# Kernel tuning notes

Hardware: AMD Instinct MI355X
Metric: run time of the kernel (lower is better)

Reference implementation:

```python
import jax, jax.numpy as jnp
import numpy as np

N, E = 50000, 800000
IN_DIM, EDGE_DIM, HID, OUT_DIM, L = 128, 16, 64, 8, 4
MSG_EPS = 1e-7  # GENConv eps added to relu(msg)


def layer_norm(x, g, b, eps=1e-5):
    mu = x.mean(-1, keepdims=True)
    var = ((x - mu) ** 2).mean(-1, keepdims=True)
    return (x - mu) * jax.lax.rsqrt(var + eps) * g + b


def segment_softmax(logits, seg, num_segments):
    # numerically stable softmax over edges grouped by destination node
    m = jax.ops.segment_max(logits, seg, num_segments=num_segments)
    m = jnp.where(jnp.isfinite(m), m, 0.0)
    e = jnp.exp(logits - m[seg])
    s = jax.ops.segment_sum(e, seg, num_segments=num_segments)
    return e / (s[seg] + 1e-16)


def gen_conv(x, src, dst, ea, t, W1, b1, g1, be1, W2, b2):
    # GENConv: message = relu(x_j + e_ij) + eps, softmax-aggregate by dst, add root, MLP [h->2h->h]
    msg = jax.nn.relu(x[src] + ea) + MSG_EPS          # [E, H]
    alpha = segment_softmax(msg * t, dst, x.shape[0]) # [E, H]
    agg = jax.ops.segment_sum(msg * alpha, dst, num_segments=x.shape[0])  # [N, H]
    h = agg + x
    h = jax.nn.relu(layer_norm(h @ W1 + b1, g1, be1))  # [N, 2H]
    return h @ W2 + b2                                 # [N, H]


def setup_inputs() -> dict:
    key = jax.random.key(0)
    ks = jax.random.split(key, 16)
    sc = 0.05
    inp = {
        "x": jax.random.normal(ks[0], (N, IN_DIM), jnp.float32),
        "edge_attr": jax.random.normal(ks[1], (E, EDGE_DIM), jnp.float32),
        "node_W": jax.random.normal(ks[2], (IN_DIM, HID), jnp.float32) * sc,
        "node_b": jnp.zeros((HID,), jnp.float32),
        "edge_W": jax.random.normal(ks[3], (EDGE_DIM, HID), jnp.float32) * sc,
        "edge_b": jnp.zeros((HID,), jnp.float32),
        "conv_t": jnp.ones((L,), jnp.float32),
        "conv_W1": jax.random.normal(ks[4], (L, HID, 2 * HID), jnp.float32) * sc,
        "conv_b1": jnp.zeros((L, 2 * HID), jnp.float32),
        "conv_g1": jnp.ones((L, 2 * HID), jnp.float32),
        "conv_be1": jnp.zeros((L, 2 * HID), jnp.float32),
        "conv_W2": jax.random.normal(ks[5], (L, 2 * HID, HID), jnp.float32) * sc,
        "conv_b2": jnp.zeros((L, HID), jnp.float32),
        "ln_g": jnp.ones((L, HID), jnp.float32),
        "ln_b": jnp.zeros((L, HID), jnp.float32),
        "lin_W": jax.random.normal(ks[6], (HID, OUT_DIM), jnp.float32) * sc,
        "lin_b": jnp.zeros((OUT_DIM,), jnp.float32),
        "edge_index": jax.random.randint(ks[7], (2, E), 0, N, jnp.int64),
    }
    return inp


def reference(x, edge_attr, node_W, node_b, edge_W, edge_b,
              conv_t, conv_W1, conv_b1, conv_g1, conv_be1, conv_W2, conv_b2,
              ln_g, ln_b, lin_W, lin_b, edge_index):
    src, dst = edge_index[0], edge_index[1]  # flow: source_to_target
    h = x @ node_W + node_b
    ea = edge_attr @ edge_W + edge_b
    # first layer: conv only (DeeperGCN applies layers[0].conv directly)
    h = gen_conv(h, src, dst, ea, conv_t[0], conv_W1[0], conv_b1[0],
                 conv_g1[0], conv_be1[0], conv_W2[0], conv_b2[0])
    # res+ blocks: x + conv(dropout(relu(norm(x)))); dropout inactive (eval)
    for i in range(1, L):
        z = jax.nn.relu(layer_norm(h, ln_g[i], ln_b[i]))
        h = h + gen_conv(z, src, dst, ea, conv_t[i], conv_W1[i], conv_b1[i],
                         conv_g1[i], conv_be1[i], conv_W2[i], conv_b2[i])
    h = jax.nn.relu(layer_norm(h, ln_g[0], ln_b[0]))
    return h @ lin_W + lin_b
```

## Files before the change

### kernel.cpp

```cpp
#include <hip/hip_runtime.h>
#include <hip/hip_fp16.h>

#define N_NODES 50000
#define N_EDGES 800000
#define IN_DIM  128
#define EDGE_DIM 16
#define HID     64
#define HID2    128
#define OUT_DIM 8
#define N_LAYERS 4
#define NBUCK   391
#define CCHUNK  4096
#define CBLOCKS 196

typedef _Float16 half8 __attribute__((ext_vector_type(8)));
typedef float floatx4 __attribute__((ext_vector_type(4)));

static __device__ __forceinline__ float bcast(float v, int l) {
    return __uint_as_float(__builtin_amdgcn_readlane(__float_as_uint(v), l));
}

__global__ __launch_bounds__(256, 4) void chist_kernel(
    const int* __restrict__ dsts, int* __restrict__ ccnt)
{
    __shared__ int lh[NBUCK];
    for (int i = threadIdx.x; i < NBUCK; i += 256) lh[i] = 0;
    __syncthreads();
    const int base = blockIdx.x * CCHUNK;
#pragma unroll
    for (int i = 0; i < 16; ++i) {
        const int e = base + i * 256 + threadIdx.x;
        if (e < N_EDGES) atomicAdd(&lh[dsts[e] >> 7], 1);
    }
    __syncthreads();
    for (int i = threadIdx.x; i < NBUCK; i += 256)
        if (lh[i]) atomicAdd(&ccnt[i], lh[i]);
}

__global__ __launch_bounds__(256, 1) void cscan_kernel(
    const int* __restrict__ ccnt, int* __restrict__ coff, int* __restrict__ ccur)
{
    __shared__ int part[512];
    const int t = threadIdx.x;
    part[t]       = (t < NBUCK)       ? ccnt[t]       : 0;
    part[t + 256] = (t + 256 < NBUCK) ? ccnt[t + 256] : 0;
    __syncthreads();
    for (int off = 1; off < 512; off <<= 1) {
        const int v0 = (t >= off) ? part[t - off] : 0;
        const int v1 = (t + 256 >= off) ? part[t + 256 - off] : 0;
        __syncthreads();
        part[t] += v0; part[t + 256] += v1;
        __syncthreads();
    }
    if (t < NBUCK) { const int ex = (t > 0) ? part[t - 1] : 0; coff[t] = ex; ccur[t] = ex; }
    const int i2 = t + 256;
    if (i2 < NBUCK) { coff[i2] = part[i2 - 1]; ccur[i2] = part[i2 - 1]; }
    if (t == 0) coff[NBUCK] = part[NBUCK - 1];
}

__global__ __launch_bounds__(256, 4) void cscatter_kernel(
    const int* __restrict__ srcs, const int* __restrict__ dsts,
    int* __restrict__ ccur, uint2* __restrict__ tmp)
{
    __shared__ int lh[NBUCK], lbase[NBUCK], lrank[NBUCK];
    for (int i = threadIdx.x; i < NBUCK; i += 256) { lh[i] = 0; lrank[i] = 0; }
    __syncthreads();
    const int base = blockIdx.x * CCHUNK;
    int myd[16], mys[16];
#pragma unroll
    for (int i = 0; i < 16; ++i) {
        const int e = base + i * 256 + threadIdx.x;
        if (e < N_EDGES) {
            myd[i] = dsts[e]; mys[i] = srcs[e];
            atomicAdd(&lh[myd[i] >> 7], 1);
        } else myd[i] = -1;
    }
    __syncthreads();
    for (int i = threadIdx.x; i < NBUCK; i += 256) {
        const int c = lh[i];
        lbase[i] = c ? atomicAdd(&ccur[i], c) : 0;
    }
    __syncthreads();
#pragma unroll
    for (int i = 0; i < 16; ++i) {
        if (myd[i] >= 0) {
            const int e = base + i * 256 + threadIdx.x;
            const int b = myd[i] >> 7;
            const int r = atomicAdd(&lrank[b], 1);
            tmp[lbase[b] + r] =
                make_uint2((unsigned)mys[i] | ((unsigned)myd[i] << 16),
                           (unsigned)e);
        }
    }
}

__global__ __launch_bounds__(256, 1) void fsort_kernel(
    const uint2* __restrict__ tmp, const int* __restrict__ coff,
    unsigned* __restrict__ sd2, int* __restrict__ eid)
{
    __shared__ uint2 ebuf[4096];
    __shared__ int lh[128], lsc[128];
    const int b = blockIdx.x;
    const int lo = coff[b];
    const int cnt = coff[b + 1] - lo;
    if (threadIdx.x < 128) lh[threadIdx.x] = 0;
    __syncthreads();
    for (int i = threadIdx.x; i < cnt; i += 256) {
        const uint2 v = tmp[lo + i];
        ebuf[i] = v;
        atomicAdd(&lh[(int)(v.x >> 16) - b * 128], 1);
    }
    __syncthreads();
    if (threadIdx.x < 128) lsc[threadIdx.x] = lh[threadIdx.x];
    __syncthreads();
    for (int off = 1; off < 128; off <<= 1) {
        int v = 0;
        if (threadIdx.x < 128 && threadIdx.x >= off) v = lsc[threadIdx.x - off];
        __syncthreads();
        if (threadIdx.x < 128) lsc[threadIdx.x] += v;
        __syncthreads();
    }
    if (threadIdx.x < 128) lh[threadIdx.x] = lsc[threadIdx.x] - lh[threadIdx.x];
    __syncthreads();
    for (int i = threadIdx.x; i < cnt; i += 256) {
        const uint2 v = ebuf[i];
        const int d = (int)(v.x >> 16) - b * 128;
        const int pos = atomicAdd(&lh[d], 1);
        sd2[lo + pos] = v.x;
        eid[lo + pos] = (int)v.y;
    }
}

__global__ __launch_bounds__(256, 2) void node_proj_kernel(
    const float* __restrict__ x, const float* __restrict__ W,
    const float* __restrict__ b, float* __restrict__ h, __half* __restrict__ zh)
{
    __shared__ float xs[4][IN_DIM];
    const int c = threadIdx.x & 63;
    const int local_n = threadIdx.x >> 6;
    float w[IN_DIM];
#pragma unroll
    for (int k = 0; k < IN_DIM; ++k) w[k] = W[k * HID + c];
    const float bias = b[c];

    for (int base = blockIdx.x * 4; base < N_NODES; base += gridDim.x * 4) {
        __syncthreads();
#pragma unroll
        for (int i = 0; i < 2; ++i) {
            int idx = threadIdx.x + i * 256;
            int nn = idx >> 7, kk = idx & 127;
            xs[nn][kk] = x[(base + nn) * IN_DIM + kk];
        }
        __syncthreads();
        const int n = base + local_n;
        float acc = bias;
#pragma unroll
        for (int k4 = 0; k4 < IN_DIM / 4; ++k4) {
            float4 xv = ((const float4*)xs[local_n])[k4];
            acc = fmaf(xv.x, w[k4 * 4 + 0], acc);
            acc = fmaf(xv.y, w[k4 * 4 + 1], acc);
            acc = fmaf(xv.z, w[k4 * 4 + 2], acc);
            acc = fmaf(xv.w, w[k4 * 4 + 3], acc);
        }
        h[n * HID + c] = acc;
        zh[n * HID + c] = __float2half(acc);
    }
}

__global__ __launch_bounds__(256, 4) void edge_emb_kernel(
    const float* __restrict__ ea, const float* __restrict__ W,
    const float* __restrict__ b, const int* __restrict__ eid,
    __half* __restrict__ eah)
{
    __shared__ __half lds_t[4][16 * HID];
    const int lane = threadIdx.x & 63;
    const int waveid = threadIdx.x >> 6;
    const int wave = (blockIdx.x * 256 + threadIdx.x) >> 6;
    const int nwaves = gridDim.x * 4;
    const int m = lane & 15, q = lane >> 4;
    const int NT = N_EDGES / 16;

    half8 bf[4];
#pragma unroll
    for (int blk = 0; blk < 4; ++blk) {
#pragma unroll
        for (int i = 0; i < 8; ++i) {
            const int k = q * 8 + i;
            bf[blk][i] = (k < EDGE_DIM)
                ? (_Float16)W[k * HID + blk * 16 + m] : (_Float16)0.f;
        }
    }
    float bv[4];
#pragma unroll
    for (int blk = 0; blk < 4; ++blk) bv[blk] = b[blk * 16 + m];

    const int ed = lane >> 3, ch = lane & 7;

    for (int tile = wave; tile < NT; tile += nwaves) {
        const int e0 = tile * 16;
        const int eidx = eid[e0 + m];
        half8 af;
#pragma unroll
        for (int i = 0; i < 8; ++i) af[i] = (_Float16)0.f;
        if (q < 2) {
            const float4* ap =
                (const float4*)(ea + (size_t)eidx * EDGE_DIM + q * 8);
            const float4 lo = ap[0];
            const float4 hi = ap[1];
            af[0] = (_Float16)lo.x; af[1] = (_Float16)lo.y;
            af[2] = (_Float16)lo.z; af[3] = (_Float16)lo.w;
            af[4] = (_Float16)hi.x; af[5] = (_Float16)hi.y;
            af[6] = (_Float16)hi.z; af[7] = (_Float16)hi.w;
        }
        floatx4 c[4];
#pragma unroll
        for (int blk = 0; blk < 4; ++blk) {
            floatx4 cin = {bv[blk], bv[blk], bv[blk], bv[blk]};
            c[blk] = __builtin_amdgcn_mfma_f32_16x16x32_f16(
                af, bf[blk], cin, 0, 0, 0);
        }
#pragma unroll
        for (int blk = 0; blk < 4; ++blk)
#pragma unroll
            for (int r = 0; r < 4; ++r)
                lds_t[waveid][(q * 4 + r) * HID + blk * 16 + m] =
                    __float2half(c[blk][r]);
        const float4 v0 =
            *(const float4*)&lds_t[waveid][ed * HID + ch * 8];
        const float4 v1 =
            *(const float4*)&lds_t[waveid][(8 + ed) * HID + ch * 8];
        ((float4*)(eah + (size_t)(e0 + ed) * HID))[ch] = v0;
        ((float4*)(eah + (size_t)(e0 + 8 + ed) * HID))[ch] = v1;
    }
}

__global__ __launch_bounds__(256, 3) void edge_agg_kernel(
    const __half* __restrict__ zh, const __half* __restrict__ eah,
    const unsigned* __restrict__ sd2,
    const float* __restrict__ conv_t, int layer,
    float2* __restrict__ ps)
{
    const int lane = threadIdx.x & 63;
    const int wave = (blockIdx.x * 256 + threadIdx.x) >> 6;
    const int nwaves = gridDim.x * 4;
    const float t2 = conv_t[layer] * 1.4426950408889634f;
    const int NT = N_EDGES / 64;

    const _Float16* zf = (const _Float16*)zh;
    const _Float16* ef = (const _Float16*)eah;

    for (int tile = wave; tile < NT; tile += nwaves) {
        const int e0 = tile * 64;
        const unsigned sdv = sd2[e0 + lane];
        const _Float16* erow = ef + (size_t)e0 * HID + lane;

        _Float16 ez[64];
#pragma unroll
        for (int k = 0; k < 64; ++k) ez[k] = erow[(size_t)k * HID];

        const int sv = (int)(sdv & 0xffffu);
        const int dv = (int)(sdv >> 16);
        const int pv = __shfl_up(dv, 1, 64);
        const unsigned long long bmask = __ballot(dv != pv) & ~1ull;

        _Float16 za[16], zb[16];
#pragma unroll
        for (int k = 0; k < 16; ++k) {
            const int a = __builtin_amdgcn_readlane(sv, k);
            za[k] = zf[(size_t)a * HID + lane];
        }

        float S = 0.f, P = 0.f;
        int cur = __builtin_amdgcn_readlane(dv, 0);
        bool first = true;
#pragma unroll
        for (int g = 0; g < 4; ++g) {
            if (g < 3) {
#pragma unroll
                for (int k = 0; k < 16; ++k) {
                    const int a = __builtin_amdgcn_readlane(sv, (g + 1) * 16 + k);
                    zb[k] = zf[(size_t)a * HID + lane];
                }
            }
#pragma unroll
            for (int k = 0; k < 16; ++k) {
                const int j = g * 16 + k;
                if (bmask & (1ull << j)) {
                    float2* addr = &ps[(size_t)cur * HID + lane];
                    if (first) {
                        unsafeAtomicAdd(&addr->x, P);
                        unsafeAtomicAdd(&addr->y, S);
                        first = false;
                    } else {
                        *addr = make_float2(P, S);
                    }
                    S = 0.f; P = 0.f;
                    cur = __builtin_amdgcn_readlane(dv, j);
                }
                _Float16 mh = za[k] + ez[j];
                mh = mh > (_Float16)0.f ? mh : (_Float16)0.f;
                const float mm = (float)mh + 1e-7f;
                const float xx = __builtin_amdgcn_exp2f(mm * t2);
                S += xx;
                P = fmaf(mm, xx, P);
            }
            if (g < 3) {
#pragma unroll
                for (int k = 0; k < 16; ++k) za[k] = zb[k];
            }
        }
        {
            float2* addr = &ps[(size_t)cur * HID + lane];
            unsafeAtomicAdd(&addr->x, P);
            unsafeAtomicAdd(&addr->y, S);
        }
    }
}

__global__ __launch_bounds__(256, 3) void node_mm1_kernel(
    float2* __restrict__ ps,
    const __half* __restrict__ zh,
    const float* __restrict__ W1, const float* __restrict__ b1,
    const float* __restrict__ g1, const float* __restrict__ be1,
    __half* __restrict__ vh)
{
    const int lane = threadIdx.x & 63;
    const int wave = (blockIdx.x * 256 + threadIdx.x) >> 6;

    float wa[HID], wb[HID];
#pragma unroll
    for (int k = 0; k < HID; ++k) {
        wa[k] = W1[k * HID2 + lane];
        wb[k] = W1[k * HID2 + 64 + lane];
    }
    const float ba = b1[lane],  bb = b1[64 + lane];
    const float ga = g1[lane],  gb = g1[64 + lane];
    const float ca = be1[lane], cb = be1[64 + lane];

    int idx[4];
    float2 pv[4];
    float zv[4];
#pragma unroll
    for (int i = 0; i < 4; ++i) idx[i] = (wave + i * 12500) * HID + lane;
#pragma unroll
    for (int i = 0; i < 4; ++i) pv[i] = ps[idx[i]];
#pragma unroll
    for (int i = 0; i < 4; ++i) zv[i] = __half2float(zh[idx[i]]);
#pragma unroll
    for (int i = 0; i < 4; ++i) ps[idx[i]] = make_float2(0.f, 0.f);
    float hv[4];
#pragma unroll
    for (int i = 0; i < 4; ++i)
        hv[i] = pv[i].x / (pv[i].y + 1e-16f) + zv[i];

#pragma unroll
    for (int pr = 0; pr < 2; ++pr) {
        const float h0 = hv[pr * 2], h1 = hv[pr * 2 + 1];
        float a0 = 0.f, a1 = 0.f, c0 = 0.f, c1 = 0.f;
        float d0 = 0.f, d1 = 0.f, e0 = 0.f, e1 = 0.f;
#pragma unroll
        for (int k = 0; k < 32; ++k) {
            const float x0 = bcast(h0, k);
            const float x1 = bcast(h0, k + 32);
            const float y0 = bcast(h1, k);
            const float y1 = bcast(h1, k + 32);
            a0 = fmaf(x0, wa[k], a0);
            c0 = fmaf(x0, wb[k], c0);
            a1 = fmaf(x1, wa[k + 32], a1);
            c1 = fmaf(x1, wb[k + 32], c1);
            d0 = fmaf(y0, wa[k], d0);
            e0 = fmaf(y0, wb[k], e0);
            d1 = fmaf(y1, wa[k + 32], d1);
            e1 = fmaf(y1, wb[k + 32], e1);
        }
        const float ua0 = (a0 + a1) + ba, ub0 = (c0 + c1) + bb;
        const float ua1 = (d0 + d1) + ba, ub1 = (e0 + e1) + bb;

        float s0 = ua0 + ub0, s1 = ua1 + ub1;
#pragma unroll
        for (int o = 1; o < 64; o <<= 1) {
            s0 += __shfl_xor(s0, o, 64);
            s1 += __shfl_xor(s1, o, 64);
        }
        const float mu0 = s0 * (1.f / 128.f), mu1 = s1 * (1.f / 128.f);
        const float da0 = ua0 - mu0, db0 = ub0 - mu0;
        const float da1 = ua1 - mu1, db1 = ub1 - mu1;
        float q0 = fmaf(da0, da0, db0 * db0);
        float q1 = fmaf(da1, da1, db1 * db1);
#pragma unroll
        for (int o = 1; o < 64; o <<= 1) {
            q0 += __shfl_xor(q0, o, 64);
            q1 += __shfl_xor(q1, o, 64);
        }
        const float r0 = rsqrtf(q0 * (1.f / 128.f) + 1e-5f);
        const float r1 = rsqrtf(q1 * (1.f / 128.f) + 1e-5f);
        const float ya0 = da0 * r0 * ga + ca, yb0 = db0 * r0 * gb + cb;
        const float ya1 = da1 * r1 * ga + ca, yb1 = db1 * r1 * gb + cb;
        const size_t v0 = (size_t)(wave + pr * 2 * 12500) * HID2;
        const size_t v1 = (size_t)(wave + (pr * 2 + 1) * 12500) * HID2;
        vh[v0 + lane]      = __float2half(ya0 > 0.f ? ya0 : 0.f);
        vh[v0 + 64 + lane] = __float2half(yb0 > 0.f ? yb0 : 0.f);
        vh[v1 + lane]      = __float2half(ya1 > 0.f ? ya1 : 0.f);
        vh[v1 + 64 + lane] = __float2half(yb1 > 0.f ? yb1 : 0.f);
    }
}

__global__ __launch_bounds__(256, 3) void node_mm2_kernel(
    const __half* __restrict__ vh,
    const float* __restrict__ W2, const float* __restrict__ b2,
    const float* __restrict__ lng, const float* __restrict__ lnb,
    float* __restrict__ h, __half* __restrict__ zh, int residual)
{
    const int lane = threadIdx.x & 63;
    const int wave = (blockIdx.x * 256 + threadIdx.x) >> 6;

    float wa[HID], wb[HID];
#pragma unroll
    for (int k = 0; k < HID; ++k) {
        wa[k] = W2[k * HID + lane];
        wb[k] = W2[(k + 64) * HID + lane];
    }
    const float bias = b2[lane];
    const float g = lng[lane];
    const float be = lnb[lane];

    int idx[4];
    float f0[4], f1[4], hold[4];
#pragma unroll
    for (int i = 0; i < 4; ++i) idx[i] = (wave + i * 12500) * HID + lane;
#pragma unroll
    for (int i = 0; i < 4; ++i) {
        const size_t vb = (size_t)(wave + i * 12500) * HID2;
        f0[i] = __half2float(vh[vb + lane]);
        f1[i] = __half2float(vh[vb + 64 + lane]);
    }
#pragma unroll
    for (int i = 0; i < 4; ++i) hold[i] = h[idx[i]];

#pragma unroll
    for (int pr = 0; pr < 2; ++pr) {
        const int i0 = pr * 2, i1 = pr * 2 + 1;
        float a0 = 0.f, a1 = 0.f, c0 = 0.f, c1 = 0.f;
        float d0 = 0.f, d1 = 0.f, e0 = 0.f, e1 = 0.f;
#pragma unroll
        for (int k = 0; k < 32; ++k) {
            a0 = fmaf(bcast(f0[i0], k),      wa[k],      a0);
            a1 = fmaf(bcast(f0[i0], k + 32), wa[k + 32], a1);
            c0 = fmaf(bcast(f1[i0], k),      wb[k],      c0);
            c1 = fmaf(bcast(f1[i0], k + 32), wb[k + 32], c1);
            d0 = fmaf(bcast(f0[i1], k),      wa[k],      d0);
            d1 = fmaf(bcast(f0[i1], k + 32), wa[k + 32], d1);
            e0 = fmaf(bcast(f1[i1], k),      wb[k],      e0);
            e1 = fmaf(bcast(f1[i1], k + 32), wb[k + 32], e1);
        }
        const float acc0 = (a0 + a1) + (c0 + c1) + bias;
        const float acc1 = (d0 + d1) + (e0 + e1) + bias;
        const float hn0 = residual ? (hold[i0] + acc0) : acc0;
        const float hn1 = residual ? (hold[i1] + acc1) : acc1;
        h[idx[i0]] = hn0;
        h[idx[i1]] = hn1;

        float s0 = hn0, s1 = hn1;
#pragma unroll
        for (int o = 1; o < 64; o <<= 1) {
            s0 += __shfl_xor(s0, o, 64);
            s1 += __shfl_xor(s1, o, 64);
        }
        const float mu0 = s0 * (1.f / 64.f), mu1 = s1 * (1.f / 64.f);
        const float dd0 = hn0 - mu0, dd1 = hn1 - mu1;
        float q0 = dd0 * dd0, q1 = dd1 * dd1;
#pragma unroll
        for (int o = 1; o < 64; o <<= 1) {
            q0 += __shfl_xor(q0, o, 64);
            q1 += __shfl_xor(q1, o, 64);
        }
        const float r0 = rsqrtf(q0 * (1.f / 64.f) + 1e-5f);
        const float r1 = rsqrtf(q1 * (1.f / 64.f) + 1e-5f);
        const float y0 = dd0 * r0 * g + be;
        const float y1 = dd1 * r1 * g + be;
        zh[idx[i0]] = __float2half(y0 > 0.f ? y0 : 0.f);
        zh[idx[i1]] = __float2half(y1 > 0.f ? y1 : 0.f);
    }
}

__global__ __launch_bounds__(256, 4) void final_kernel(
    const __half* __restrict__ zh, const float* __restrict__ Wl,
    const float* __restrict__ bl, float* __restrict__ out)
{
    __shared__ float wl[HID * OUT_DIM];
    for (int i = threadIdx.x; i < HID * OUT_DIM; i += 256) wl[i] = Wl[i];
    __syncthreads();
    const int total = N_NODES * OUT_DIM;
    for (int idx = blockIdx.x * 256 + threadIdx.x; idx < total;
         idx += gridDim.x * 256) {
        const int n = idx >> 3, o = idx & 7;
        const __half2* zp = (const __half2*)(zh + (size_t)n * HID);
        float acc = bl[o];
#pragma unroll
        for (int k2 = 0; k2 < HID / 2; ++k2) {
            const float2 f = __half22float2(zp[k2]);
            acc = fmaf(f.x, wl[(k2 * 2 + 0) * OUT_DIM + o], acc);
            acc = fmaf(f.y, wl[(k2 * 2 + 1) * OUT_DIM + o], acc);
        }
        out[idx] = acc;
    }
}

extern "C" void kernel_launch(void* const* d_in, const int* in_sizes, int n_in,
                              void* d_out, int out_size, void* d_ws, size_t ws_size,
                              hipStream_t stream)
{
    const float* x         = (const float*)d_in[0];
    const float* edge_attr = (const float*)d_in[1];
    const float* node_W    = (const float*)d_in[2];
    const float* node_b    = (const float*)d_in[3];
    const float* edge_W    = (const float*)d_in[4];
    const float* edge_b    = (const float*)d_in[5];
    const float* conv_t    = (const float*)d_in[6];
    const float* conv_W1   = (const float*)d_in[7];
    const float* conv_b1   = (const float*)d_in[8];
    const float* conv_g1   = (const float*)d_in[9];
    const float* conv_be1  = (const float*)d_in[10];
    const float* conv_W2   = (const float*)d_in[11];
    const float* conv_b2   = (const float*)d_in[12];
    const float* ln_g      = (const float*)d_in[13];
    const float* ln_b      = (const float*)d_in[14];
    const float* lin_W     = (const float*)d_in[15];
    const float* lin_b     = (const float*)d_in[16];
    const int*   edge_index= (const int*)d_in[17];
    const int*   srcs = edge_index;
    const int*   dsts = edge_index + N_EDGES;
    float* out = (float*)d_out;

    float* h    = (float*)d_ws;
    float2* ps  = (float2*)(h + N_NODES * HID);
    __half* vh  = (__half*)(ps + N_NODES * HID);
    __half* zh  = vh + (size_t)N_NODES * HID2;
    __half* eah = zh + (size_t)N_NODES * HID;
    uint2* tmp  = (uint2*)(eah + (size_t)N_EDGES * HID);
    unsigned* sd2 = (unsigned*)(tmp + N_EDGES);
    int* eid    = (int*)(sd2 + N_EDGES);
    int* ccnt   = eid + N_EDGES;
    int* coff   = ccnt + NBUCK;
    int* ccur   = coff + NBUCK + 1;

    hipMemsetAsync(ccnt, 0, (size_t)NBUCK * sizeof(int), stream);
    chist_kernel<<<CBLOCKS, 256, 0, stream>>>(dsts, ccnt);
    cscan_kernel<<<1, 256, 0, stream>>>(ccnt, coff, ccur);
    cscatter_kernel<<<CBLOCKS, 256, 0, stream>>>(srcs, dsts, ccur, tmp);
    fsort_kernel<<<NBUCK, 256, 0, stream>>>(tmp, coff, sd2, eid);

    node_proj_kernel<<<2048, 256, 0, stream>>>(x, node_W, node_b, h, zh);
    edge_emb_kernel<<<3125, 256, 0, stream>>>(edge_attr, edge_W, edge_b, eid, eah);

    hipMemsetAsync(ps, 0, (size_t)N_NODES * HID * sizeof(float2), stream);

    for (int layer = 0; layer < N_LAYERS; ++layer) {
        edge_agg_kernel<<<3125, 256, 0, stream>>>(zh, eah, sd2,
                                                  conv_t, layer, ps);
        node_mm1_kernel<<<3125, 256, 0, stream>>>(
            ps, zh,
            conv_W1 + (size_t)layer * HID * HID2, conv_b1 + layer * HID2,
            conv_g1 + layer * HID2, conv_be1 + layer * HID2, vh);
        const float* gz = (layer < N_LAYERS - 1) ? (ln_g + (layer + 1) * HID) : ln_g;
        const float* bz = (layer < N_LAYERS - 1) ? (ln_b + (layer + 1) * HID) : ln_b;
        node_mm2_kernel<<<3125, 256, 0, stream>>>(
            vh, conv_W2 + (size_t)layer * HID2 * HID, conv_b2 + layer * HID,
            gz, bz, h, zh, layer > 0 ? 1 : 0);
    }
    final_kernel<<<1024, 256, 0, stream>>>(zh, lin_W, lin_b, out);
}
```

Measured before the change: 640.9 us.

## Prefetch next edge tile in edge_agg and rewrite node_proj with lane broadcasts

The edge aggregation kernel now runs as a persistent grid of fewer blocks, with each wave loading the next tile's edge embeddings and packed indices into registers while it computes the current tile. This is meant to hide global load latency behind the exp/accumulate work, at the cost of much higher register pressure from a second 64-element buffer, which could spill or lower occupancy. The node projection kernel drops its LDS staging and block barriers. Each wave now handles four fixed nodes loaded straight into registers and broadcasts x values across lanes with readlane, using a larger grid and a higher occupancy hint.

```diff
diff --git a/kernel.cpp b/kernel.cpp
--- a/kernel.cpp
+++ b/kernel.cpp
@@ -131,39 +131,44 @@
     }
 }
 
-__global__ __launch_bounds__(256, 2) void node_proj_kernel(
+__global__ __launch_bounds__(256, 3) void node_proj_kernel(
     const float* __restrict__ x, const float* __restrict__ W,
     const float* __restrict__ b, float* __restrict__ h, __half* __restrict__ zh)
 {
-    __shared__ float xs[4][IN_DIM];
-    const int c = threadIdx.x & 63;
-    const int local_n = threadIdx.x >> 6;
+    const int lane = threadIdx.x & 63;
+    const int wave = (blockIdx.x * 256 + threadIdx.x) >> 6;
+
     float w[IN_DIM];
 #pragma unroll
-    for (int k = 0; k < IN_DIM; ++k) w[k] = W[k * HID + c];
-    const float bias = b[c];
-
-    for (int base = blockIdx.x * 4; base < N_NODES; base += gridDim.x * 4) {
-        __syncthreads();
-#pragma unroll
-        for (int i = 0; i < 2; ++i) {
-            int idx = threadIdx.x + i * 256;
-            int nn = idx >> 7, kk = idx & 127;
-            xs[nn][kk] = x[(base + nn) * IN_DIM + kk];
-        }
-        __syncthreads();
-        const int n = base + local_n;
-        float acc = bias;
-#pragma unroll
-        for (int k4 = 0; k4 < IN_DIM / 4; ++k4) {
-            float4 xv = ((const float4*)xs[local_n])[k4];
-            acc = fmaf(xv.x, w[k4 * 4 + 0], acc);
-            acc = fmaf(xv.y, w[k4 * 4 + 1], acc);
-            acc = fmaf(xv.z, w[k4 * 4 + 2], acc);
-            acc = fmaf(xv.w, w[k4 * 4 + 3], acc);
-        }
-        h[n * HID + c] = acc;
-        zh[n * HID + c] = __float2half(acc);
+    for (int k = 0; k < IN_DIM; ++k) w[k] = W[k * HID + lane];
+    const float bias = b[lane];
+
+    float xa[4], xb[4];
+#pragma unroll
+    for (int i = 0; i < 4; ++i) {
+        const size_t xbase = (size_t)(wave + i * 12500) * IN_DIM;
+        xa[i] = x[xbase + lane];
+        xb[i] = x[xbase + 64 + lane];
+    }
+
+#pragma unroll
+    for (int pr = 0; pr < 2; ++pr) {
+        const int i0 = pr * 2, i1 = pr * 2 + 1;
+        float a0 = 0.f, a1 = 0.f, d0 = 0.f, d1 = 0.f;
+#pragma unroll
+        for (int k = 0; k < 64; ++k) {
+            a0 = fmaf(bcast(xa[i0], k), w[k],      a0);
+            a1 = fmaf(bcast(xb[i0], k), w[k + 64], a1);
+            d0 = fmaf(bcast(xa[i1], k), w[k],      d0);
+            d1 = fmaf(bcast(xb[i1], k), w[k + 64], d1);
+        }
+        const float u0 = (a0 + a1) + bias;
+        const float u1 = (d0 + d1) + bias;
+        const int n0 = wave + i0 * 12500, n1 = wave + i1 * 12500;
+        h[n0 * HID + lane] = u0;
+        zh[n0 * HID + lane] = __float2half(u0);
+        h[n1 * HID + lane] = u1;
+        zh[n1 * HID + lane] = __float2half(u1);
     }
 }
 
@@ -241,7 +246,6 @@
     float2* __restrict__ ps)
 {
     const int lane = threadIdx.x & 63;
-    const int wave = (blockIdx.x * 256 + threadIdx.x) >> 6;
     const int nwaves = gridDim.x * 4;
     const float t2 = conv_t[layer] * 1.4426950408889634f;
     const int NT = N_EDGES / 64;
@@ -249,14 +253,27 @@
     const _Float16* zf = (const _Float16*)zh;
     const _Float16* ef = (const _Float16*)eah;
 
-    for (int tile = wave; tile < NT; tile += nwaves) {
-        const int e0 = tile * 64;
-        const unsigned sdv = sd2[e0 + lane];
-        const _Float16* erow = ef + (size_t)e0 * HID + lane;
-
-        _Float16 ez[64];
+    int tile = (blockIdx.x * 256 + threadIdx.x) >> 6;
+    if (tile >= NT) return;
+
+    unsigned sdv = sd2[tile * 64 + lane];
+    _Float16 ez[64];
+    {
+        const _Float16* erow = ef + (size_t)tile * 64 * HID + lane;
 #pragma unroll
         for (int k = 0; k < 64; ++k) ez[k] = erow[(size_t)k * HID];
+    }
+
+    while (true) {
+        const int nxt = tile + nwaves;
+        unsigned sdv_n = 0;
+        _Float16 ezn[64];
+        if (nxt < NT) {
+            sdv_n = sd2[nxt * 64 + lane];
+            const _Float16* erown = ef + (size_t)nxt * 64 * HID + lane;
+#pragma unroll
+            for (int k = 0; k < 64; ++k) ezn[k] = erown[(size_t)k * HID];
+        }
 
         const int sv = (int)(sdv & 0xffffu);
         const int dv = (int)(sdv >> 16);
@@ -314,6 +331,12 @@
             unsafeAtomicAdd(&addr->x, P);
             unsafeAtomicAdd(&addr->y, S);
         }
+
+        if (nxt >= NT) break;
+        tile = nxt;
+        sdv = sdv_n;
+#pragma unroll
+        for (int k = 0; k < 64; ++k) ez[k] = ezn[k];
     }
 }
 
@@ -550,14 +573,14 @@
     cscatter_kernel<<<CBLOCKS, 256, 0, stream>>>(srcs, dsts, ccur, tmp);
     fsort_kernel<<<NBUCK, 256, 0, stream>>>(tmp, coff, sd2, eid);
 
-    node_proj_kernel<<<2048, 256, 0, stream>>>(x, node_W, node_b, h, zh);
+    node_proj_kernel<<<3125, 256, 0, stream>>>(x, node_W, node_b, h, zh);
     edge_emb_kernel<<<3125, 256, 0, stream>>>(edge_attr, edge_W, edge_b, eid, eah);
 
     hipMemsetAsync(ps, 0, (size_t)N_NODES * HID * sizeof(float2), stream);
 
     for (int layer = 0; layer < N_LAYERS; ++layer) {
-        edge_agg_kernel<<<3125, 256, 0, stream>>>(zh, eah, sd2,
-                                                  conv_t, layer, ps);
+        edge_agg_kernel<<<782, 256, 0, stream>>>(zh, eah, sd2,
+                                                 conv_t, layer, ps);
         node_mm1_kernel<<<3125, 256, 0, stream>>>(
             ps, zh,
             conv_W1 + (size_t)layer * HID * HID2, conv_b1 + layer * HID2,
```

Result: slower. 737.9 us (+15.1%).
